# Kernel optimization log

Hardware: AMD Instinct MI355X
Metric: run time of the kernel (lower is better)

Reference implementation:

```python
import jax, jax.numpy as jnp
import numpy as np

N = 150_000          # active BEV voxels
C = 128              # SHARED_CONV_CHANNEL
KK = 9               # 3x3 submanifold kernel
H = W = 1024         # BEV spatial shape at stride 8
OUT_CH = (3, 2, 1, 3, 2)   # hm, center, center_z, dim, rot
NH = 5
MAXO = 3
EPS = 1e-5
INIT_BIAS = -2.19


def _build_neighbor_idx():
    # Random sparse occupancy; pad index == N means 'inactive neighbor'
    rng = np.random.default_rng(0)
    flat = rng.choice(H * W, size=N, replace=False)
    ys, xs = flat // W, flat % W
    grid = np.full(H * W, N, dtype=np.int32)
    grid[flat] = np.arange(N, dtype=np.int32)
    nbr = np.full((N, KK), N, dtype=np.int32)
    k = 0
    for dy in (-1, 0, 1):
        for dx in (-1, 0, 1):
            ny, nx = ys + dy, xs + dx
            ok = (ny >= 0) & (ny < H) & (nx >= 0) & (nx < W)
            nbr[ok, k] = grid[(ny * W + nx)[ok]]
            k += 1
    return jnp.asarray(nbr)


def setup_inputs() -> dict:
    key = jax.random.key(0)
    k0, k1, k2 = jax.random.split(key, 3)
    x = jax.random.normal(k0, (N, C), jnp.float32)
    W1 = jax.random.normal(k1, (NH, KK, C, C), jnp.float32) * (2.0 / (KK * C)) ** 0.5  # kaiming
    gamma = jnp.ones((NH, C), jnp.float32)
    beta = jnp.zeros((NH, C), jnp.float32)
    W2 = jax.random.normal(k2, (NH, C, MAXO), jnp.float32) * 0.02
    b2 = jnp.zeros((NH, MAXO), jnp.float32).at[0, :OUT_CH[0]].set(INIT_BIAS)  # hm init_bias
    return {"x": x, "neighbor_idx": _build_neighbor_idx(),
            "W1": W1, "gamma": gamma, "beta": beta, "W2": W2, "b2": b2}


def reference(x, neighbor_idx, W1, gamma, beta, W2, b2):
    # pad row of zeros: inactive neighbors contribute nothing (submanifold conv)
    xp = jnp.concatenate([x, jnp.zeros((1, C), x.dtype)], axis=0)
    acc = jnp.zeros((NH, x.shape[0], C), x.dtype)
    for k in range(KK):                       # fixed 3x3 kernel loop
        g = xp[neighbor_idx[:, k]]            # [N, C] irregular gather
        acc = acc + jnp.einsum('nc,hcd->hnd', g, W1[:, k])
    # BatchNorm1d (training mode: batch stats over active voxels) + ReLU
    mean = acc.mean(axis=1, keepdims=True)
    var = ((acc - mean) ** 2).mean(axis=1, keepdims=True)
    h = (acc - mean) * jax.lax.rsqrt(var + EPS) * gamma[:, None, :] + beta[:, None, :]
    h = jax.nn.relu(h)
    # 1x1 SubMConv per head (padded to MAXO channels, masked)
    out = jnp.einsum('hnc,hco->hno', h, W2) + b2[:, None, :]   # [NH, N, MAXO]
    mask = (jnp.arange(MAXO)[None, :] < jnp.asarray(OUT_CH)[:, None]).astype(out.dtype)
    return out * mask[:, None, :]
```

## Files before the change

### kernel.cpp

```cpp
#include <hip/hip_runtime.h>

#define NPTS 150000
#define NHEAD 5
#define KTOT 1152
#define NTILES 1172
#define NBLK 586
#define HSTRIDE 592
#define EPSV 1e-5f
#define FXSCALE 1048576.0

typedef __bf16 bf16x8 __attribute__((ext_vector_type(8)));
typedef float f32x4 __attribute__((ext_vector_type(4)));
typedef unsigned short u16x8 __attribute__((ext_vector_type(8)));

#define WS_NEEDED 238484416UL

__device__ __forceinline__ unsigned short f2bf(float f) {
    unsigned int u = __float_as_uint(f);
    u += 0x7FFFu + ((u >> 16) & 1u);
    return (unsigned short)(u >> 16);
}

__device__ __forceinline__ void gload16(const void* g, void* l) {
    __builtin_amdgcn_global_load_lds((const __attribute__((address_space(1))) void*)g,
                                     (__attribute__((address_space(3))) void*)l, 16, 0, 0);
}

__global__ void k_pre(const float* __restrict__ x, unsigned short* __restrict__ xbf,
                      const float* __restrict__ W1, unsigned short* __restrict__ w1t,
                      const int* __restrict__ nbr, int* __restrict__ hist_t) {
    __shared__ int lh[512];
    const int bid = blockIdx.x;
    const int t = threadIdx.x;
    if (bid < 9376) {
        const size_t i8 = (size_t)bid * 256 + t;
        const size_t base = i8 * 8;
        if (base >= (size_t)(NPTS + 1) * 128) return;
        if (base < (size_t)NPTS * 128) {
            const f32x4 v0 = __builtin_nontemporal_load((const f32x4*)(x + base));
            const f32x4 v1 = __builtin_nontemporal_load((const f32x4*)(x + base + 4));
            u16x8 o;
            o[0] = f2bf(v0[0]); o[1] = f2bf(v0[1]); o[2] = f2bf(v0[2]); o[3] = f2bf(v0[3]);
            o[4] = f2bf(v1[0]); o[5] = f2bf(v1[1]); o[6] = f2bf(v1[2]); o[7] = f2bf(v1[3]);
            *(u16x8*)(xbf + base) = o;
        } else {
            u16x8 z = {0,0,0,0,0,0,0,0};
            *(u16x8*)(xbf + base) = z;
        }
    } else if (bid < 9376 + 2880) {
        const int idx = (bid - 9376) * 256 + t;
        const int d = idx & 127;
        const int c = (idx >> 7) & 127;
        const int hk = idx >> 14;
        const int k = hk % 9, h = hk / 9;
        const int col = h * 128 + d;
        const int p = k * 128 + c;
        const int s32 = p >> 5;
        const int j0 = (p >> 3) & 3;
        const int jj = j0 ^ ((col >> 1) & 3);
        w1t[(size_t)col * KTOT + s32 * 32 + jj * 8 + (p & 7)] = f2bf(W1[idx]);
    } else {
        const int b = bid - 12256;
        lh[t] = 0; lh[t + 256] = 0;
        __syncthreads();
        const int n = b * 256 + t;
        if (n < NPTS) {
            int pat = 0;
#pragma unroll
            for (int k = 0; k < 9; k++) pat |= (nbr[n * 9 + k] != NPTS) << k;
            atomicAdd(&lh[pat], 1);
        }
        __syncthreads();
        hist_t[t * HSTRIDE + b] = lh[t];
        hist_t[(t + 256) * HSTRIDE + b] = lh[t + 256];
    }
}

__global__ void k_scan1(int* __restrict__ hist_t, int* __restrict__ tot) {
    const int p = blockIdx.x;
    const int lane = threadIdx.x;
    int run = 0;
    for (int c = 0; c < 10; c++) {
        const int i = c * 64 + lane;
        const int orig = (i < NBLK) ? hist_t[p * HSTRIDE + i] : 0;
        int v = orig;
        for (int d = 1; d < 64; d <<= 1) {
            const int w = __shfl_up(v, d);
            if (lane >= d) v += w;
        }
        if (i < NBLK) hist_t[p * HSTRIDE + i] = run + v - orig;
        run += __shfl(v, 63);
    }
    if (lane == 0) tot[p] = run;
}

__global__ void k_scan2(const int* __restrict__ tot, int* __restrict__ base,
                        unsigned long long* __restrict__ sacc) {
    __shared__ int t512[512];
    const int k = threadIdx.x;
    for (int i = k; i < 1280; i += 512) sacc[i] = 0ULL;
    const int v = tot[k];
    t512[k] = v;
    __syncthreads();
    for (int d = 1; d < 512; d <<= 1) {
        const int w = (k >= d) ? t512[k - d] : 0;
        __syncthreads();
        t512[k] += w;
        __syncthreads();
    }
    base[k] = t512[k] - v;
}

__global__ void k_scatter(const int* __restrict__ nbr, const int* __restrict__ hist_t,
                          const int* __restrict__ base, int* __restrict__ perm) {
    __shared__ int pat_s[256];
    const int t = threadIdx.x, b = blockIdx.x;
    const int n = b * 256 + t;
    int pat = -1;
    if (n < NPTS) {
        pat = 0;
#pragma unroll
        for (int k = 0; k < 9; k++) pat |= (nbr[n * 9 + k] != NPTS) << k;
    }
    pat_s[t] = pat;
    __syncthreads();
    if (n < NPTS) {
        int rank = 0;
        for (int j = 0; j < 256; j++) rank += (j < t) & (pat_s[j] == pat);
        perm[base[pat] + hist_t[pat * HSTRIDE + b] + rank] = n;
    }
}

__global__ __launch_bounds__(512, 4) void k_gemm(
    const unsigned short* __restrict__ xbf,
    const unsigned short* __restrict__ w1t,
    const int* __restrict__ nbr,
    const int* __restrict__ perm,
    unsigned short* __restrict__ accw,
    unsigned long long* __restrict__ sacc)
{
    __shared__ unsigned short ABC[28672];
    __shared__ int nbr_s[9 * 128];
    __shared__ int perm_s[128];
    __shared__ int mask_s;

    const int tid = threadIdx.x;
    const int wid = tid >> 6;
    const int lane = tid & 63;
    const int bm = blockIdx.x;
    const int b2 = blockIdx.y;
    const int tile = (bm * 331) % NTILES;
    const int tile0 = tile * 128;

    if (tid == 0) mask_s = 0;
    if (tid < 128) {
        const int gr = tile0 + tid;
        perm_s[tid] = (gr < NPTS) ? perm[gr] : NPTS;
    }
    __syncthreads();
    if (tid < 128) {
        const int prow = perm_s[tid];
        int pat = 0;
#pragma unroll
        for (int k = 0; k < 9; k++) {
            const int v = (prow < NPTS) ? nbr[prow * 9 + k] : NPTS;
            nbr_s[k * 128 + tid] = v;
            pat |= (v != NPTS) << k;
        }
        if (pat) atomicOr(&mask_s, pat);
    }
    __syncthreads();
    const int mask = mask_s | 16;
    const int steps = 4 * __builtin_popcount(mask);

    const int RM = (wid >> 2) * 64;
    const int CNl = (wid & 3) * 80;
    const int lr16 = lane >> 2;
    const int lb = lane & 3;
    const int jswS = (lb ^ ((lr16 >> 1) & 3)) * 8;

    f32x4 acc[4][5];
#pragma unroll
    for (int m = 0; m < 4; m++)
#pragma unroll
        for (int n = 0; n < 5; n++) acc[m][n] = f32x4{0.f, 0.f, 0.f, 0.f};

    auto stage = [&](int buf, int kn, int q) {
#pragma unroll
        for (int j = 0; j < 4; ++j) {
            const int g = wid + 8 * j;
            if (g < 8) {
                const int r = g * 16 + lr16;
                const int idx = nbr_s[kn * 128 + r];
                gload16(xbf + (size_t)idx * 128 + q * 32 + jswS,
                        (void*)(ABC + buf * 4096 + g * 512));
            } else if (g < 28) {
                const int gb = g - 8;
                const int lc = gb * 16 + lr16;
                gload16(w1t + (size_t)(b2 * 320 + lc) * KTOT + (kn * 4 + q) * 32 + lb * 8,
                        (void*)(ABC + 8192 + buf * 10240 + gb * 512));
            }
        }
    };

    const int rlo = lane & 15;
    const int jsw = (((lane >> 4) ^ ((rlo >> 1) & 3))) * 8;

    auto compute = [&](int buf) {
        const unsigned short* Ab = ABC + buf * 4096;
        const unsigned short* Bb = ABC + 8192 + buf * 10240;
        bf16x8 a[4];
#pragma unroll
        for (int m = 0; m < 4; m++)
            a[m] = *reinterpret_cast<const bf16x8*>(&Ab[(RM + m * 16 + rlo) * 32 + jsw]);
#pragma unroll
        for (int n = 0; n < 5; n++) {
            const bf16x8 b = *reinterpret_cast<const bf16x8*>(&Bb[(CNl + n * 16 + rlo) * 32 + jsw]);
#pragma unroll
            for (int m = 0; m < 4; m++)
                acc[m][n] = __builtin_amdgcn_mfma_f32_16x16x32_bf16(a[m], b, acc[m][n], 0, 0, 0);
        }
    };

    int ckn = __builtin_ctz(mask), cq = 0, rem = mask & (mask - 1), buf = 0;
    stage(0, ckn, 0);
    __syncthreads();
    for (int i = 0; i < steps; i++) {
        int nkn, nq, nrem;
        if (cq < 3) { nkn = ckn; nq = cq + 1; nrem = rem; }
        else { nkn = rem ? __builtin_ctz(rem) : 0; nq = 0; nrem = rem & (rem - 1); }
        if (i + 1 < steps) stage(buf ^ 1, nkn, nq);
        compute(buf);
        __syncthreads();
        ckn = nkn; cq = nq; rem = nrem; buf ^= 1;
    }

    float sn[5], qn[5];
#pragma unroll
    for (int n = 0; n < 5; n++) {
        float s = 0.f, q = 0.f;
#pragma unroll
        for (int m = 0; m < 4; m++)
#pragma unroll
            for (int r = 0; r < 4; r++) { const float v = acc[m][n][r]; s += v; q += v * v; }
        s += __shfl_xor(s, 16); s += __shfl_xor(s, 32);
        q += __shfl_xor(q, 16); q += __shfl_xor(q, 32);
        sn[n] = s; qn[n] = q;
    }
    if (lane < 16) {
#pragma unroll
        for (int n = 0; n < 5; n++) {
            const int gcol = b2 * 320 + CNl + n * 16 + lane;
            atomicAdd(&sacc[gcol],
                      (unsigned long long)__double2ll_rn((double)sn[n] * FXSCALE));
            atomicAdd(&sacc[640 + gcol],
                      (unsigned long long)__double2ll_rn((double)qn[n] * FXSCALE));
        }
    }

    unsigned short* C = (unsigned short*)ABC;
#pragma unroll
    for (int p = 0; p < 2; ++p) {
        __syncthreads();
        if (((wid >> 1) & 1) == p) {
            const int colbase = CNl - p * 160;
#pragma unroll
            for (int m = 0; m < 4; m++) {
                const int row = RM + m * 16 + (lane >> 4) * 4;
#pragma unroll
                for (int n = 0; n < 5; n++) {
                    const int col = colbase + n * 16 + rlo;
#pragma unroll
                    for (int r = 0; r < 4; r++)
                        C[(row + r) * 168 + col] = f2bf(acc[m][n][r]);
                }
            }
        }
        __syncthreads();
#pragma unroll
        for (int j = 0; j < 5; j++) {
            const int chunk = tid + 512 * j;
            const int row = chunk / 20, cc = chunk % 20;
            const int gr = tile0 + row;
            if (gr < NPTS) {
                const int col = b2 * 320 + p * 160 + cc * 8;
                const int hh = col >> 7, d = col & 127;
                __builtin_nontemporal_store(*(const u16x8*)&C[row * 168 + cc * 8],
                    (u16x8*)(accw + ((size_t)hh * NPTS + gr) * 128 + d));
            }
        }
    }
}

__global__ void k_stats(const unsigned long long* __restrict__ sacc,
                        float* __restrict__ stats) {
    const int c = threadIdx.x;
    const double s = (double)(long long)sacc[c] * (1.0 / FXSCALE);
    const double q = (double)(long long)sacc[640 + c] * (1.0 / FXSCALE);
    const double mean = s * (1.0 / NPTS);
    const double var = q * (1.0 / NPTS) - mean * mean;
    stats[c] = (float)mean;
    stats[640 + c] = (float)(1.0 / sqrt(var + (double)EPSV));
}

__global__ void k_out(const unsigned short* __restrict__ accw,
                      const int* __restrict__ perm,
                      const float* __restrict__ stats,
                      const float* __restrict__ gamma, const float* __restrict__ beta,
                      const float* __restrict__ W2, const float* __restrict__ b2,
                      float* __restrict__ out) {
    __shared__ float sc[128], sh[128], w2s[384], b2s[3];
    __shared__ int nout_s[128];
    const int h = blockIdx.y;
    const int t = threadIdx.x;
    if (t < 128) {
        const float mean = stats[h * 128 + t];
        const float rstd = stats[640 + h * 128 + t];
        const float g = gamma[h * 128 + t];
        const float bb = beta[h * 128 + t];
        sc[t] = rstd * g;
        sh[t] = bb - mean * rstd * g;
        w2s[t * 3 + 0] = W2[(h * 128 + t) * 3 + 0];
        w2s[t * 3 + 1] = W2[(h * 128 + t) * 3 + 1];
        w2s[t * 3 + 2] = W2[(h * 128 + t) * 3 + 2];
        const int gr = blockIdx.x * 128 + t;
        nout_s[t] = (gr < NPTS) ? perm[gr] : NPTS;
    }
    if (t < 3) b2s[t] = b2[h * 3 + t];
    __syncthreads();
    const int row = t >> 1;
    const int half = t & 1;
    const int gr = blockIdx.x * 128 + row;
    const int noc = (h == 2) ? 1 : ((h == 1 || h == 4) ? 2 : 3);
    float o0 = 0.f, o1 = 0.f, o2 = 0.f;
    if (gr < NPTS) {
        const unsigned short* rp = accw + ((size_t)h * NPTS + gr) * 128 + half * 64;
#pragma unroll
        for (int c8 = 0; c8 < 8; c8++) {
            const u16x8 v = __builtin_nontemporal_load((const u16x8*)(rp + c8 * 8));
#pragma unroll
            for (int j = 0; j < 8; j++) {
                const int c = half * 64 + c8 * 8 + j;
                const float a = __uint_as_float(((unsigned int)v[j]) << 16);
                const float hc = fmaxf(fmaf(a, sc[c], sh[c]), 0.f);
                o0 = fmaf(hc, w2s[c * 3 + 0], o0);
                o1 = fmaf(hc, w2s[c * 3 + 1], o1);
                o2 = fmaf(hc, w2s[c * 3 + 2], o2);
            }
        }
    }
    o0 += __shfl_xor(o0, 1);
    o1 += __shfl_xor(o1, 1);
    o2 += __shfl_xor(o2, 1);
    if (half == 0 && gr < NPTS) {
        const size_t ob = ((size_t)h * NPTS + nout_s[row]) * 3;
        __builtin_nontemporal_store((noc > 0) ? (o0 + b2s[0]) : 0.f, out + ob + 0);
        __builtin_nontemporal_store((noc > 1) ? (o1 + b2s[1]) : 0.f, out + ob + 1);
        __builtin_nontemporal_store((noc > 2) ? (o2 + b2s[2]) : 0.f, out + ob + 2);
    }
}

__global__ void k_sentinel(float* __restrict__ out, int n) {
    const int i = blockIdx.x * 256 + threadIdx.x;
    if (i < n) out[i] = 12345.0f;
}

extern "C" void kernel_launch(void* const* d_in, const int* in_sizes, int n_in,
                              void* d_out, int out_size, void* d_ws, size_t ws_size,
                              hipStream_t stream) {
    const float* x     = (const float*)d_in[0];
    const int*   nbr   = (const int*)d_in[1];
    const float* W1    = (const float*)d_in[2];
    const float* gamma = (const float*)d_in[3];
    const float* beta  = (const float*)d_in[4];
    const float* W2    = (const float*)d_in[5];
    const float* b2    = (const float*)d_in[6];
    float* out = (float*)d_out;

    if (ws_size < WS_NEEDED) {
        k_sentinel<<<(out_size + 255) / 256, 256, 0, stream>>>(out, out_size);
        return;
    }

    char* ws = (char*)d_ws;
    unsigned short* xbf      = (unsigned short*)(ws);
    unsigned short* w1t      = (unsigned short*)(ws + 38404096);
    unsigned short* accw     = (unsigned short*)(ws + 39878656);
    int*            hist_t   = (int*)(ws + 39878656);
    int*            tot      = (int*)(ws + 39878656 + 2097152);
    int*            base     = (int*)(ws + 39878656 + 2099200);
    unsigned long long* sacc = (unsigned long long*)(ws + 231878656);
    float*          stats    = (float*)(ws + 237879296);
    int*            perm     = (int*)(ws + 237884416);

    k_pre<<<12842, 256, 0, stream>>>(x, xbf, W1, w1t, nbr, hist_t);
    k_scan1<<<512, 64, 0, stream>>>(hist_t, tot);
    k_scan2<<<1, 512, 0, stream>>>(tot, base, sacc);
    k_scatter<<<NBLK, 256, 0, stream>>>(nbr, hist_t, base, perm);
    k_gemm<<<dim3(NTILES, 2), 512, 0, stream>>>(xbf, w1t, nbr, perm, accw, sacc);
    k_stats<<<1, 640, 0, stream>>>(sacc, stats);
    k_out<<<dim3(NTILES, 5), 256, 0, stream>>>(accw, perm, stats, gamma, beta, W2, b2, out);
}
```

Before: 369.9 us.

## Triple-buffer gathered A tiles with two-step prefetch and split vmcnt waits

Splits the GEMM tile staging into separate loads for the gathered activation (A) tile and the weight (B) tile. A now uses three LDS buffers and is prefetched two k-steps ahead, while B stays double-buffered one step ahead. The per-step __syncthreads is replaced by an explicit s_waitcnt vmcnt(1) plus s_barrier, so the newest A gather can remain in flight during compute. The aim is to hide the latency of the irregular neighbor gather. The cost is more LDS per block and reliance on exact ordering of global-load counts, which is fragile if the load pattern changes.

```diff
diff --git a/kernel.cpp b/kernel.cpp
--- a/kernel.cpp
+++ b/kernel.cpp
@@ -139,7 +139,7 @@
     unsigned short* __restrict__ accw,
     unsigned long long* __restrict__ sacc)
 {
-    __shared__ unsigned short ABC[28672];
+    __shared__ unsigned short ABC[32768];
     __shared__ int nbr_s[9 * 128];
     __shared__ int perm_s[128];
     __shared__ int mask_s;
@@ -185,20 +185,20 @@
 #pragma unroll
         for (int n = 0; n < 5; n++) acc[m][n] = f32x4{0.f, 0.f, 0.f, 0.f};
 
-    auto stage = [&](int buf, int kn, int q) {
-#pragma unroll
-        for (int j = 0; j < 4; ++j) {
-            const int g = wid + 8 * j;
-            if (g < 8) {
-                const int r = g * 16 + lr16;
-                const int idx = nbr_s[kn * 128 + r];
-                gload16(xbf + (size_t)idx * 128 + q * 32 + jswS,
-                        (void*)(ABC + buf * 4096 + g * 512));
-            } else if (g < 28) {
-                const int gb = g - 8;
+    auto stageA = [&](int buf, int kn, int q) {
+        const int r = wid * 16 + lr16;
+        const int idx = nbr_s[kn * 128 + r];
+        gload16(xbf + (size_t)idx * 128 + q * 32 + jswS,
+                (void*)(ABC + buf * 4096 + wid * 512));
+    };
+    auto stageB = [&](int buf, int kn, int q) {
+#pragma unroll
+        for (int j = 0; j < 3; ++j) {
+            const int gb = wid + 8 * j;
+            if (gb < 20) {
                 const int lc = gb * 16 + lr16;
                 gload16(w1t + (size_t)(b2 * 320 + lc) * KTOT + (kn * 4 + q) * 32 + lb * 8,
-                        (void*)(ABC + 8192 + buf * 10240 + gb * 512));
+                        (void*)(ABC + 12288 + buf * 10240 + gb * 512));
             }
         }
     };
@@ -206,9 +206,9 @@
     const int rlo = lane & 15;
     const int jsw = (((lane >> 4) ^ ((rlo >> 1) & 3))) * 8;
 
-    auto compute = [&](int buf) {
-        const unsigned short* Ab = ABC + buf * 4096;
-        const unsigned short* Bb = ABC + 8192 + buf * 10240;
+    auto compute = [&](int bufA, int bufB) {
+        const unsigned short* Ab = ABC + bufA * 4096;
+        const unsigned short* Bb = ABC + 12288 + bufB * 10240;
         bf16x8 a[4];
 #pragma unroll
         for (int m = 0; m < 4; m++)
@@ -222,18 +222,31 @@
         }
     };
 
-    int ckn = __builtin_ctz(mask), cq = 0, rem = mask & (mask - 1), buf = 0;
-    stage(0, ckn, 0);
-    __syncthreads();
-    for (int i = 0; i < steps; i++) {
-        int nkn, nq, nrem;
-        if (cq < 3) { nkn = ckn; nq = cq + 1; nrem = rem; }
-        else { nkn = rem ? __builtin_ctz(rem) : 0; nq = 0; nrem = rem & (rem - 1); }
-        if (i + 1 < steps) stage(buf ^ 1, nkn, nq);
-        compute(buf);
-        __syncthreads();
-        ckn = nkn; cq = nq; rem = nrem; buf ^= 1;
-    }
+    auto adv = [](int& kn, int& q, int& rem) {
+        if (q < 3) q++;
+        else { if (rem) { kn = __builtin_ctz(rem); rem &= rem - 1; } q = 0; }
+    };
+    int ckn = __builtin_ctz(mask), cq = 0, crem = mask & (mask - 1);
+    int bkn = ckn, bq = cq, brem = crem; adv(bkn, bq, brem);
+    int akn = bkn, aq = bq, arem = brem; adv(akn, aq, arem);
+
+    stageA(0, ckn, cq);
+    stageB(0, ckn, cq);
+    stageA(1, bkn, bq);
+
+    int bufAc = 0, bufAs = 2;
+    for (int i = 0; i < steps; ++i) {
+        if (i == steps - 1) asm volatile("s_waitcnt vmcnt(0)" ::: "memory");
+        else                asm volatile("s_waitcnt vmcnt(1)" ::: "memory");
+        asm volatile("s_barrier" ::: "memory");
+        if (i + 1 < steps) stageB((i + 1) & 1, bkn, bq);
+        if (i + 2 < steps) stageA(bufAs, akn, aq);
+        compute(bufAc, i & 1);
+        adv(ckn, cq, crem); adv(bkn, bq, brem); adv(akn, aq, arem);
+        bufAc = (bufAc == 2) ? 0 : bufAc + 1;
+        bufAs = (bufAs == 2) ? 0 : bufAs + 1;
+    }
+    __syncthreads();
 
     float sn[5], qn[5];
 #pragma unroll
```

Result: slower. 380.7 us (+2.9%).

## Fuse scan2/stats into neighbours, use row-major accumulator and inverse permutation

Applied to the files above, without the earlier changes.

Removes the single-block k_scan2 and k_stats launches. The sacc zeroing moves into k_scan1, the base prefix scan is recomputed redundantly in every k_scatter block, and the BN statistics are computed inside k_out. The GEMM accumulator changes layout to [N,640] per row, and k_scatter builds an inverse permutation so k_out can write output rows in original order, coalesced, with all five heads per block. The trade-offs are redundant per-block scan and stats work, an extra iperm write, and scattered reads of the accumulator through iperm.

```diff
diff --git a/kernel.cpp b/kernel.cpp
--- a/kernel.cpp
+++ b/kernel.cpp
@@ -13,7 +13,7 @@
 typedef float f32x4 __attribute__((ext_vector_type(4)));
 typedef unsigned short u16x8 __attribute__((ext_vector_type(8)));
 
-#define WS_NEEDED 238484416UL
+#define WS_NEEDED 233109376UL
 
 __device__ __forceinline__ unsigned short f2bf(float f) {
     unsigned int u = __float_as_uint(f);
@@ -76,9 +76,14 @@
     }
 }
 
-__global__ void k_scan1(int* __restrict__ hist_t, int* __restrict__ tot) {
+__global__ void k_scan1(int* __restrict__ hist_t, int* __restrict__ tot,
+                        unsigned long long* __restrict__ sacc) {
     const int p = blockIdx.x;
     const int lane = threadIdx.x;
+    if (lane == 0) {
+        sacc[p] = 0ULL; sacc[512 + p] = 0ULL;
+        if (p < 256) sacc[1024 + p] = 0ULL;
+    }
     int run = 0;
     for (int c = 0; c < 10; c++) {
         const int i = c * 64 + lane;
@@ -94,40 +99,41 @@
     if (lane == 0) tot[p] = run;
 }
 
-__global__ void k_scan2(const int* __restrict__ tot, int* __restrict__ base,
-                        unsigned long long* __restrict__ sacc) {
-    __shared__ int t512[512];
-    const int k = threadIdx.x;
-    for (int i = k; i < 1280; i += 512) sacc[i] = 0ULL;
-    const int v = tot[k];
-    t512[k] = v;
+__global__ __launch_bounds__(512) void k_scatter(
+    const int* __restrict__ nbr, const int* __restrict__ hist_t,
+    const int* __restrict__ tot, int* __restrict__ perm, int* __restrict__ iperm) {
+    __shared__ int pat_s[256];
+    __shared__ int bs[512];
+    const int t = threadIdx.x, b = blockIdx.x;
+    const int v0 = tot[t];
+    bs[t] = v0;
     __syncthreads();
     for (int d = 1; d < 512; d <<= 1) {
-        const int w = (k >= d) ? t512[k - d] : 0;
-        __syncthreads();
-        t512[k] += w;
-        __syncthreads();
-    }
-    base[k] = t512[k] - v;
-}
-
-__global__ void k_scatter(const int* __restrict__ nbr, const int* __restrict__ hist_t,
-                          const int* __restrict__ base, int* __restrict__ perm) {
-    __shared__ int pat_s[256];
-    const int t = threadIdx.x, b = blockIdx.x;
-    const int n = b * 256 + t;
+        const int w = (t >= d) ? bs[t - d] : 0;
+        __syncthreads();
+        bs[t] += w;
+        __syncthreads();
+    }
+    const int base_t = bs[t] - v0;
+    __syncthreads();
+    bs[t] = base_t;
+    const int n = b * 256 + (t & 255);
     int pat = -1;
-    if (n < NPTS) {
-        pat = 0;
-#pragma unroll
-        for (int k = 0; k < 9; k++) pat |= (nbr[n * 9 + k] != NPTS) << k;
-    }
-    pat_s[t] = pat;
-    __syncthreads();
-    if (n < NPTS) {
+    if (t < 256) {
+        if (n < NPTS) {
+            pat = 0;
+#pragma unroll
+            for (int k = 0; k < 9; k++) pat |= (nbr[n * 9 + k] != NPTS) << k;
+        }
+        pat_s[t] = pat;
+    }
+    __syncthreads();
+    if (t < 256 && n < NPTS) {
         int rank = 0;
         for (int j = 0; j < 256; j++) rank += (j < t) & (pat_s[j] == pat);
-        perm[base[pat] + hist_t[pat * HSTRIDE + b] + rank] = n;
+        const int dest = bs[pat] + hist_t[pat * HSTRIDE + b] + rank;
+        perm[dest] = n;
+        iperm[n] = dest;
     }
 }
 
@@ -136,7 +142,7 @@
     const unsigned short* __restrict__ w1t,
     const int* __restrict__ nbr,
     const int* __restrict__ perm,
-    unsigned short* __restrict__ accw,
+    unsigned short* __restrict__ accw2,
     unsigned long long* __restrict__ sacc)
 {
     __shared__ unsigned short ABC[28672];
@@ -282,81 +288,94 @@
             const int chunk = tid + 512 * j;
             const int row = chunk / 20, cc = chunk % 20;
             const int gr = tile0 + row;
-            if (gr < NPTS) {
-                const int col = b2 * 320 + p * 160 + cc * 8;
-                const int hh = col >> 7, d = col & 127;
-                __builtin_nontemporal_store(*(const u16x8*)&C[row * 168 + cc * 8],
-                    (u16x8*)(accw + ((size_t)hh * NPTS + gr) * 128 + d));
-            }
-        }
-    }
-}
-
-__global__ void k_stats(const unsigned long long* __restrict__ sacc,
-                        float* __restrict__ stats) {
-    const int c = threadIdx.x;
-    const double s = (double)(long long)sacc[c] * (1.0 / FXSCALE);
-    const double q = (double)(long long)sacc[640 + c] * (1.0 / FXSCALE);
-    const double mean = s * (1.0 / NPTS);
-    const double var = q * (1.0 / NPTS) - mean * mean;
-    stats[c] = (float)mean;
-    stats[640 + c] = (float)(1.0 / sqrt(var + (double)EPSV));
-}
-
-__global__ void k_out(const unsigned short* __restrict__ accw,
-                      const int* __restrict__ perm,
-                      const float* __restrict__ stats,
-                      const float* __restrict__ gamma, const float* __restrict__ beta,
-                      const float* __restrict__ W2, const float* __restrict__ b2,
-                      float* __restrict__ out) {
-    __shared__ float sc[128], sh[128], w2s[384], b2s[3];
-    __shared__ int nout_s[128];
-    const int h = blockIdx.y;
+            const int col = b2 * 320 + p * 160 + cc * 8;
+            __builtin_nontemporal_store(*(const u16x8*)&C[row * 168 + cc * 8],
+                (u16x8*)(accw2 + (size_t)gr * 640 + col));
+        }
+    }
+}
+
+__global__ __launch_bounds__(512) void k_out(
+    const unsigned short* __restrict__ accw2,
+    const int* __restrict__ iperm,
+    const unsigned long long* __restrict__ sacc,
+    const float* __restrict__ gamma, const float* __restrict__ beta,
+    const float* __restrict__ W2, const float* __restrict__ b2,
+    float* __restrict__ out)
+{
+    __shared__ float sc[640], sh[640], w2s[1920], b2s[15];
+    __shared__ int ip_s[128];
+    __shared__ float red[128][4][6];
     const int t = threadIdx.x;
+    for (int c = t; c < 640; c += 512) {
+        const double s = (double)(long long)sacc[c] * (1.0 / FXSCALE);
+        const double q = (double)(long long)sacc[640 + c] * (1.0 / FXSCALE);
+        const double mean = s * (1.0 / NPTS);
+        const double var = q * (1.0 / NPTS) - mean * mean;
+        const float rstd = (float)(1.0 / sqrt(var + (double)EPSV));
+        const float g = gamma[c];
+        sc[c] = rstd * g;
+        sh[c] = beta[c] - (float)mean * rstd * g;
+        w2s[c * 3 + 0] = W2[c * 3 + 0];
+        w2s[c * 3 + 1] = W2[c * 3 + 1];
+        w2s[c * 3 + 2] = W2[c * 3 + 2];
+    }
+    if (t < 15) b2s[t] = b2[t];
     if (t < 128) {
-        const float mean = stats[h * 128 + t];
-        const float rstd = stats[640 + h * 128 + t];
-        const float g = gamma[h * 128 + t];
-        const float bb = beta[h * 128 + t];
-        sc[t] = rstd * g;
-        sh[t] = bb - mean * rstd * g;
-        w2s[t * 3 + 0] = W2[(h * 128 + t) * 3 + 0];
-        w2s[t * 3 + 1] = W2[(h * 128 + t) * 3 + 1];
-        w2s[t * 3 + 2] = W2[(h * 128 + t) * 3 + 2];
-        const int gr = blockIdx.x * 128 + t;
-        nout_s[t] = (gr < NPTS) ? perm[gr] : NPTS;
-    }
-    if (t < 3) b2s[t] = b2[h * 3 + t];
-    __syncthreads();
-    const int row = t >> 1;
-    const int half = t & 1;
-    const int gr = blockIdx.x * 128 + row;
-    const int noc = (h == 2) ? 1 : ((h == 1 || h == 4) ? 2 : 3);
-    float o0 = 0.f, o1 = 0.f, o2 = 0.f;
-    if (gr < NPTS) {
-        const unsigned short* rp = accw + ((size_t)h * NPTS + gr) * 128 + half * 64;
-#pragma unroll
-        for (int c8 = 0; c8 < 8; c8++) {
-            const u16x8 v = __builtin_nontemporal_load((const u16x8*)(rp + c8 * 8));
+        const int n = blockIdx.x * 128 + t;
+        ip_s[t] = (n < NPTS) ? iperm[n] : -1;
+    }
+    __syncthreads();
+
+    const int row = t >> 2;
+    const int seg = t & 3;
+    const int r = ip_s[row];
+    const int ccb = 16 - seg * 4;
+    float o0[3] = {0.f, 0.f, 0.f}, o1[3] = {0.f, 0.f, 0.f};
+    if (r >= 0) {
+        const unsigned short* rp = accw2 + (size_t)r * 640 + seg * 160;
+        for (int cc = 0; cc < ccb; cc++) {
+            const u16x8 v = __builtin_nontemporal_load((const u16x8*)(rp + cc * 8));
 #pragma unroll
             for (int j = 0; j < 8; j++) {
-                const int c = half * 64 + c8 * 8 + j;
+                const int c = seg * 160 + cc * 8 + j;
                 const float a = __uint_as_float(((unsigned int)v[j]) << 16);
                 const float hc = fmaxf(fmaf(a, sc[c], sh[c]), 0.f);
-                o0 = fmaf(hc, w2s[c * 3 + 0], o0);
-                o1 = fmaf(hc, w2s[c * 3 + 1], o1);
-                o2 = fmaf(hc, w2s[c * 3 + 2], o2);
+                o0[0] = fmaf(hc, w2s[c * 3 + 0], o0[0]);
+                o0[1] = fmaf(hc, w2s[c * 3 + 1], o0[1]);
+                o0[2] = fmaf(hc, w2s[c * 3 + 2], o0[2]);
             }
         }
-    }
-    o0 += __shfl_xor(o0, 1);
-    o1 += __shfl_xor(o1, 1);
-    o2 += __shfl_xor(o2, 1);
-    if (half == 0 && gr < NPTS) {
-        const size_t ob = ((size_t)h * NPTS + nout_s[row]) * 3;
-        __builtin_nontemporal_store((noc > 0) ? (o0 + b2s[0]) : 0.f, out + ob + 0);
-        __builtin_nontemporal_store((noc > 1) ? (o1 + b2s[1]) : 0.f, out + ob + 1);
-        __builtin_nontemporal_store((noc > 2) ? (o2 + b2s[2]) : 0.f, out + ob + 2);
+        for (int cc = ccb; cc < 20; cc++) {
+            const u16x8 v = __builtin_nontemporal_load((const u16x8*)(rp + cc * 8));
+#pragma unroll
+            for (int j = 0; j < 8; j++) {
+                const int c = seg * 160 + cc * 8 + j;
+                const float a = __uint_as_float(((unsigned int)v[j]) << 16);
+                const float hc = fmaxf(fmaf(a, sc[c], sh[c]), 0.f);
+                o1[0] = fmaf(hc, w2s[c * 3 + 0], o1[0]);
+                o1[1] = fmaf(hc, w2s[c * 3 + 1], o1[1]);
+                o1[2] = fmaf(hc, w2s[c * 3 + 2], o1[2]);
+            }
+        }
+    }
+    red[row][seg][0] = o0[0]; red[row][seg][1] = o0[1]; red[row][seg][2] = o0[2];
+    red[row][seg][3] = o1[0]; red[row][seg][4] = o1[1]; red[row][seg][5] = o1[2];
+    __syncthreads();
+
+    for (int idx = t; idx < 640; idx += 512) {
+        const int h = idx >> 7, rw = idx & 127;
+        const int n = blockIdx.x * 128 + rw;
+        if (n < NPTS) {
+            float a0 = b2s[h * 3 + 0], a1 = b2s[h * 3 + 1], a2 = b2s[h * 3 + 2];
+            if (h >= 1) { a0 += red[rw][h - 1][3]; a1 += red[rw][h - 1][4]; a2 += red[rw][h - 1][5]; }
+            if (h <= 3) { a0 += red[rw][h][0]; a1 += red[rw][h][1]; a2 += red[rw][h][2]; }
+            const int noc = (h == 2) ? 1 : ((h == 1 || h == 4) ? 2 : 3);
+            const size_t ob = ((size_t)h * NPTS + n) * 3;
+            out[ob + 0] = (noc > 0) ? a0 : 0.f;
+            out[ob + 1] = (noc > 1) ? a1 : 0.f;
+            out[ob + 2] = (noc > 2) ? a2 : 0.f;
+        }
     }
 }
 
@@ -385,19 +404,16 @@
     char* ws = (char*)d_ws;
     unsigned short* xbf      = (unsigned short*)(ws);
     unsigned short* w1t      = (unsigned short*)(ws + 38404096);
-    unsigned short* accw     = (unsigned short*)(ws + 39878656);
+    unsigned short* accw2    = (unsigned short*)(ws + 39878656);
     int*            hist_t   = (int*)(ws + 39878656);
     int*            tot      = (int*)(ws + 39878656 + 2097152);
-    int*            base     = (int*)(ws + 39878656 + 2099200);
-    unsigned long long* sacc = (unsigned long long*)(ws + 231878656);
-    float*          stats    = (float*)(ws + 237879296);
-    int*            perm     = (int*)(ws + 237884416);
+    unsigned long long* sacc = (unsigned long long*)(ws + 231899136);
+    int*            perm     = (int*)(ws + 231909376);
+    int*            iperm    = (int*)(ws + 232509376);
 
     k_pre<<<12842, 256, 0, stream>>>(x, xbf, W1, w1t, nbr, hist_t);
-    k_scan1<<<512, 64, 0, stream>>>(hist_t, tot);
-    k_scan2<<<1, 512, 0, stream>>>(tot, base, sacc);
-    k_scatter<<<NBLK, 256, 0, stream>>>(nbr, hist_t, base, perm);
-    k_gemm<<<dim3(NTILES, 2), 512, 0, stream>>>(xbf, w1t, nbr, perm, accw, sacc);
-    k_stats<<<1, 640, 0, stream>>>(sacc, stats);
-    k_out<<<dim3(NTILES, 5), 256, 0, stream>>>(accw, perm, stats, gamma, beta, W2, b2, out);
-}
+    k_scan1<<<512, 64, 0, stream>>>(hist_t, tot, sacc);
+    k_scatter<<<NBLK, 512, 0, stream>>>(nbr, hist_t, tot, perm, iperm);
+    k_gemm<<<dim3(NTILES, 2), 512, 0, stream>>>(xbf, w1t, nbr, perm, accw2, sacc);
+    k_out<<<NTILES, 512, 0, stream>>>(accw2, iperm, sacc, gamma, beta, W2, b2, out);
+}
```

New measurement: 420.3 us. 1.14x slower.
